# Kernel tuning notes

Hardware: AMD Instinct MI355X
Metric: run time of the kernel (lower is better)

The kernel has to match this reference:

```python
import jax, jax.numpy as jnp
import numpy as np

NEG = -1e20

def _rope(x):
    # x: (N, L, H, D). Original buffers use inv_freq over D with D/2 entries;
    # sin/cos tiled to full D to broadcast (original code's einsum was under-specified for 4D).
    L, D = x.shape[1], x.shape[3]
    inv_freq = 1.0 / (10000.0 ** (jnp.arange(0, D, 2, dtype=jnp.float32) / D))
    t = jnp.arange(L, dtype=jnp.float32)
    freqs = t[:, None] * inv_freq[None, :]            # (L, D/2)
    sin = jnp.concatenate([jnp.sin(freqs)] * 2, -1)[None, :, None, :]  # (1,L,1,D)
    cos = jnp.concatenate([jnp.cos(freqs)] * 2, -1)[None, :, None, :]
    return x * cos + jnp.flip(x, -1) * sin

def setup_inputs() -> dict:
    key = jax.random.key(0)
    ks = jax.random.split(key, 8)
    N, L, E, H = 2, 1024, 2048, 16
    D = E // H
    s = 0.02
    return {
        "values": jax.random.normal(ks[0], (N, L, E), jnp.float32),
        "keys": jax.random.normal(ks[1], (N, L, E), jnp.float32),
        "queries": jax.random.normal(ks[2], (N, L, E), jnp.float32),
        "mask": jax.random.randint(ks[3], (N, 1, L, L), 0, 2, jnp.int32),
        "Wv": jax.random.normal(ks[4], (D, D), jnp.float32) * s,
        "Wk": jax.random.normal(ks[5], (D, D), jnp.float32) * s,
        "Wq": jax.random.normal(ks[6], (D, D), jnp.float32) * s,
        "Wo": jax.random.normal(ks[7], (E, E), jnp.float32) * s,
        "bo": jnp.zeros((E,), jnp.float32),
    }

def reference(values, keys, queries, mask, Wv, Wk, Wq, Wo, bo):
    N, L, E = queries.shape
    H = 16
    D = E // H
    v = values.reshape(N, L, H, D)
    k = keys.reshape(N, L, H, D)
    q = queries.reshape(N, L, H, D)
    q = _rope(q)
    k = _rope(k)
    # per-head linears (nn.Linear: x @ W.T)
    v = jnp.einsum('nlhd,od->nlho', v, Wv)
    k = jnp.einsum('nlhd,od->nlho', k, Wk)
    q = jnp.einsum('nlhd,od->nlho', q, Wq)
    energy = jnp.einsum('nqhd,nkhd->nhqk', q, k)
    energy = jnp.where(mask == 0, NEG, energy)
    attn = jax.nn.softmax(energy / jnp.sqrt(jnp.float32(E)), axis=3)
    out = jnp.einsum('nhqk,nkhd->nqhd', attn, v).reshape(N, L, E)
    return out @ Wo.T + bo
```

## Files before the change

kernel.cpp:

```cpp
#include <hip/hip_runtime.h>

#define LQ 1024
#define EMB 2048
#define NH 16
#define HD 128
#define RSCALE 0.022097086912079608f

typedef unsigned short u16x8 __attribute__((ext_vector_type(8)));
typedef __bf16 bf16x8 __attribute__((ext_vector_type(8)));
typedef float f32x4 __attribute__((ext_vector_type(4)));
typedef short s16x4 __attribute__((ext_vector_type(4)));

typedef const __attribute__((address_space(1))) unsigned int* gas_t;
typedef __attribute__((address_space(3))) unsigned int* las_t;

__device__ __forceinline__ void glds16(const void* g, void* l){
  __builtin_amdgcn_global_load_lds((gas_t)g, (las_t)l, 16, 0, 0);
}
__device__ __forceinline__ unsigned short f2b(float f){
  unsigned int x = __float_as_uint(f);
  return (unsigned short)((x + 0x7fffu + ((x >> 16) & 1u)) >> 16);
}
__device__ __forceinline__ unsigned short f2bu(float f){
  union { __bf16 h; unsigned short u; } c; c.h = (__bf16)f; return c.u;
}
__device__ __forceinline__ short f2bs(float f){
  union { __bf16 h; short s; } c; c.h = (__bf16)f; return c.s;
}
__device__ __forceinline__ bf16x8 as_bf(u16x8 u){
  union { u16x8 u; bf16x8 b; } c; c.u = u; return c.b;
}
__device__ __forceinline__ f32x4 mfma16(s16x4 a, s16x4 b, f32x4 c){
  return __builtin_amdgcn_mfma_f32_16x16x16bf16_1k(a, b, c, 0, 0, 0);
}

__global__ __launch_bounds__(256) void k_proj(
    const float* __restrict__ vals, const float* __restrict__ keys,
    const float* __restrict__ qrys,
    const float* __restrict__ Wv, const float* __restrict__ Wk,
    const float* __restrict__ Wq,
    const float* __restrict__ Wo, const int* __restrict__ M,
    unsigned short* __restrict__ kp, unsigned short* __restrict__ qp,
    unsigned short* __restrict__ vtF, unsigned short* __restrict__ Wob,
    unsigned long long* __restrict__ Mb)
{
  __shared__ unsigned short Xs[64 * 136];
  __shared__ unsigned short Ws[128 * 136];
  __shared__ float scC[16 * 128], scS[16 * 128];
  int t = threadIdx.x;
  int which = blockIdx.y;

  if (which == 3) {
    int bx = blockIdx.x;
    #pragma unroll 4
    for (int k = 0; k < 32; ++k) {
      int i = (bx * 8192 + k * 256 + t) * 4;
      float4 f = *(const float4*)&Wo[i];
      ushort4 u;
      u.x = f2bu(f.x); u.y = f2bu(f.y); u.z = f2bu(f.z); u.w = f2bu(f.w);
      *(ushort4*)&Wob[i] = u;
    }
    int w = t >> 6, lane = t & 63;
    for (int i0 = 0; i0 < 64; i0 += 8) {
      int v[8];
      #pragma unroll
      for (int j = 0; j < 8; ++j) {
        int w_idx = bx * 256 + w * 64 + i0 + j;
        int n = w_idx >> 14, row = (w_idx >> 4) & 1023, wc = w_idx & 15;
        v[j] = M[(size_t)n * (LQ * LQ) + (size_t)row * LQ + wc * 64 + lane];
      }
      #pragma unroll
      for (int j = 0; j < 8; ++j) {
        unsigned long long b = __ballot(v[j] != 0);
        if (lane == 0) Mb[bx * 256 + w * 64 + i0 + j] = b;
      }
    }
    return;
  }

  const float* X; const float* W; bool rope;
  if (which == 0)      { X = vals; W = Wv; rope = false; }
  else if (which == 1) { X = keys; W = Wk; rope = true;  }
  else                 { X = qrys; W = Wq; rope = true;  }
  float qs = (which == 2) ? RSCALE : 1.0f;

  int w = t >> 6, lane = t & 63, quad = lane >> 4, n16 = lane & 15;

  #pragma unroll
  for (int i = 0; i < 8; ++i) {
    int ci = t + 256 * i;
    int row = ci >> 4, ch = ci & 15;
    float4 a = *(const float4*)&W[row * 128 + ch * 8];
    float4 b = *(const float4*)&W[row * 128 + ch * 8 + 4];
    u16x8 u;
    u[0]=f2bu(a.x); u[1]=f2bu(a.y); u[2]=f2bu(a.z); u[3]=f2bu(a.w);
    u[4]=f2bu(b.x); u[5]=f2bu(b.y); u[6]=f2bu(b.z); u[7]=f2bu(b.w);
    *(u16x8*)&Ws[row * 136 + ch * 8] = u;
  }
  if (rope) {
    int l0 = (blockIdx.x * 16) & 1023;
    #pragma unroll
    for (int i = 0; i < 8; ++i) {
      int idx = t + 256 * i;
      int li = idx >> 7, d = idx & 127, j = d & 63;
      float inv = 1.0f / powf(10000.0f, (float)(2 * j) * 0.0078125f);
      float ang = (float)(l0 + li) * inv;
      scC[idx] = cosf(ang);
      scS[idx] = sinf(ang);
    }
  }
  __syncthreads();

  int bh0 = blockIdx.x >> 2;
  for (int tile = 0; tile < 4; ++tile) {
    int bx4 = blockIdx.x * 4 + tile;
    int m0 = bx4 * 64;
    int kt0 = bx4 & 15;

    if (which == 0) {
      int n = bh0 >> 4, h = bh0 & 15;
      #pragma unroll
      for (int i = 0; i < 8; ++i) {
        int fi = t + 256 * i;
        int row = fi >> 5, dq = (fi & 31) * 4;
        size_t gr = (size_t)n * 16384 + (size_t)(kt0 * 64 + row) * 16 + h;
        float4 x = *(const float4*)&X[gr * HD + dq];
        ushort4 u;
        u.x = f2bu(x.x); u.y = f2bu(x.y); u.z = f2bu(x.z); u.w = f2bu(x.w);
        *(ushort4*)&Xs[row * 136 + dq] = u;
      }
    } else {
      #pragma unroll
      for (int i = 0; i < 8; ++i) {
        int fi = t + 256 * i;
        int row = fi >> 5, dq = (fi & 31) * 4;
        int gr = m0 + row;
        float4 x = *(const float4*)&X[(size_t)gr * HD + dq];
        int li = tile * 4 + (row >> 4);
        float4 xm = *(const float4*)&X[(size_t)gr * HD + (124 - dq)];
        float4 c  = *(const float4*)&scC[li * 128 + dq];
        float4 s  = *(const float4*)&scS[li * 128 + dq];
        ushort4 u;
        u.x = f2bu(x.x * c.x + xm.w * s.x);
        u.y = f2bu(x.y * c.y + xm.z * s.y);
        u.z = f2bu(x.z * c.z + xm.y * s.z);
        u.w = f2bu(x.w * c.w + xm.x * s.w);
        *(ushort4*)&Xs[row * 136 + dq] = u;
      }
    }
    __syncthreads();

    f32x4 of[4][2];
    #pragma unroll
    for (int a = 0; a < 4; ++a)
      { of[a][0] = (f32x4){0.f,0.f,0.f,0.f}; of[a][1] = (f32x4){0.f,0.f,0.f,0.f}; }

    #pragma unroll
    for (int kd = 0; kd < 4; ++kd) {
      bf16x8 bfr[2];
      #pragma unroll
      for (int b2 = 0; b2 < 2; ++b2)
        bfr[b2] = as_bf(*(const u16x8*)&Ws[(w * 32 + b2 * 16 + n16) * 136 + kd * 32 + quad * 8]);
      #pragma unroll
      for (int a = 0; a < 4; ++a) {
        bf16x8 af = as_bf(*(const u16x8*)&Xs[(a * 16 + n16) * 136 + kd * 32 + quad * 8]);
        of[a][0] = __builtin_amdgcn_mfma_f32_16x16x32_bf16(af, bfr[0], of[a][0], 0, 0, 0);
        of[a][1] = __builtin_amdgcn_mfma_f32_16x16x32_bf16(af, bfr[1], of[a][1], 0, 0, 0);
      }
    }

    if (which == 0) {
      size_t vbase = (size_t)bh0 * (LQ * HD) + (size_t)kt0 * 8192;
      #pragma unroll
      for (int a = 0; a < 4; ++a) {
        u16x8 u;
        u[0]=f2bu(of[a][0][0]); u[1]=f2bu(of[a][0][1]);
        u[2]=f2bu(of[a][0][2]); u[3]=f2bu(of[a][0][3]);
        u[4]=f2bu(of[a][1][0]); u[5]=f2bu(of[a][1][1]);
        u[6]=f2bu(of[a][1][2]); u[7]=f2bu(of[a][1][3]);
        *(u16x8*)&vtF[vbase + (size_t)(((a * 4 + w) * 64 + (quad * 16 + n16)) * 8)] = u;
      }
      __syncthreads();
    } else {
      unsigned short* OUT = (which == 1) ? kp : qp;
      __syncthreads();
      #pragma unroll
      for (int a = 0; a < 4; ++a)
        #pragma unroll
        for (int b2 = 0; b2 < 2; ++b2)
          #pragma unroll
          for (int r = 0; r < 4; ++r)
            Xs[(a * 16 + quad * 4 + r) * 136 + w * 32 + b2 * 16 + n16] =
                f2bu(of[a][b2][r] * qs);
      __syncthreads();
      #pragma unroll
      for (int i = 0; i < 4; ++i) {
        int chunk = t + 256 * i;
        int row = chunk >> 4, dc = chunk & 15;
        u16x8 v = *(const u16x8*)&Xs[row * 136 + dc * 8];
        int m = m0 + row;
        int n = m >> 14, l = (m >> 4) & 1023, h = m & 15;
        *(u16x8*)&OUT[(((size_t)(n * NH + h)) * LQ + l) * HD + dc * 8] = v;
      }
      __syncthreads();
    }
  }
}

__global__ __launch_bounds__(512) void k_attn(
    const unsigned short* __restrict__ qp, const unsigned short* __restrict__ kp,
    const unsigned short* __restrict__ vtF, const unsigned long long* __restrict__ Mb,
    unsigned short* __restrict__ ao)
{
  __shared__ unsigned short KsF[2][8192];
  __shared__ unsigned short VsF[2][8192];
  __shared__ float ls[8][16];
  int t = threadIdx.x, w = t >> 6, lane = t & 63, quad = lane >> 4, n16 = lane & 15;
  int grp = w >> 2, wq = w & 3;
  int lin = blockIdx.y * gridDim.x + blockIdx.x;
  int xcd = lin & 7, j = lin >> 3;
  int bh = xcd + 8 * (j >> 4);
  int q0 = (j & 15) * 64;
  int nIdx = bh >> 4, h = bh & 15;
  size_t base = (size_t)bh * LQ * HD;
  const unsigned short* Q = qp + base;
  const unsigned short* K = kp + base;
  const unsigned short* VF = vtF + base;

  bf16x8 qf[4];
  #pragma unroll
  for (int kd = 0; kd < 4; ++kd)
    qf[kd] = as_bf(*(const u16x8*)&Q[(size_t)(q0 + wq * 16 + n16) * HD + kd * 32 + quad * 8]);

  const unsigned long long* MbRow =
      Mb + ((size_t)nIdx * LQ + q0 + wq * 16 + n16) * 16;

  f32x4 of[8];
  #pragma unroll
  for (int c = 0; c < 8; ++c) of[c] = (f32x4){0.f, 0.f, 0.f, 0.f};
  float lp = 0.f;

  for (int p = 0; p < 8; ++p) {
    int k0 = p * 128;
    __syncthreads();
    #pragma unroll
    for (int jj = 0; jj < 2; ++jj) {
      int kt = 2 * p + jj;
      #pragma unroll
      for (int i = 0; i < 2; ++i) {
        int D = t + 512 * i;
        int nn = D & 15, qq = (D >> 4) & 3, cc = (D >> 6) & 3, kd = D >> 8;
        glds16(&K[(size_t)(k0 + jj * 64 + cc * 16 + nn) * HD + (kd * 4 + qq) * 8],
               &KsF[jj][(size_t)D * 8]);
        glds16(&VF[(size_t)kt * 8192 + (size_t)D * 8],
               &VsF[jj][(size_t)D * 8]);
      }
    }
    unsigned long long mq = MbRow[2 * p + grp];
    __syncthreads();

    unsigned long long msh = mq >> (quad * 4);

    f32x4 sf[4];
    #pragma unroll
    for (int c = 0; c < 4; ++c) sf[c] = (f32x4){0.f, 0.f, 0.f, 0.f};
    __builtin_amdgcn_s_setprio(1);
    #pragma unroll
    for (int kd = 0; kd < 4; ++kd) {
      #pragma unroll
      for (int c = 0; c < 4; ++c) {
        bf16x8 kv = as_bf(*(const u16x8*)&KsF[grp][((kd * 4 + c) * 64 + lane) * 8]);
        sf[c] = __builtin_amdgcn_mfma_f32_16x16x32_bf16(kv, qf[kd], sf[c], 0, 0, 0);
      }
    }
    __builtin_amdgcn_s_setprio(0);
    #pragma unroll
    for (int c = 0; c < 4; ++c) {
      s16x4 pa;
      #pragma unroll
      for (int r = 0; r < 4; ++r) {
        int bit = (int)((msh >> (c * 16 + r)) & 1ull);
        float p = bit ? __expf(sf[c][r]) : 0.f;
        lp += p;
        pa[r] = f2bs(p);
      }
      __builtin_amdgcn_s_setprio(1);
      #pragma unroll
      for (int c2p = 0; c2p < 4; ++c2p) {
        u16x8 vv2 = *(const u16x8*)&VsF[grp][((c * 4 + c2p) * 64 + lane) * 8];
        s16x4 vlo = { (short)vv2[0], (short)vv2[1], (short)vv2[2], (short)vv2[3] };
        s16x4 vhi = { (short)vv2[4], (short)vv2[5], (short)vv2[6], (short)vv2[7] };
        of[2 * c2p]     = mfma16(pa, vlo, of[2 * c2p]);
        of[2 * c2p + 1] = mfma16(pa, vhi, of[2 * c2p + 1]);
      }
      __builtin_amdgcn_s_setprio(0);
    }
  }

  __syncthreads();
  {
    float s = lp;
    s += __shfl_xor(s, 16);
    s += __shfl_xor(s, 32);
    ls[w][n16] = s;
  }
  float* OF = (float*)&KsF[0][0];
  unsigned short* AO = &VsF[0][0];
  if (grp == 1) {
    #pragma unroll
    for (int c2 = 0; c2 < 8; ++c2) {
      #pragma unroll
      for (int r = 0; r < 4; ++r) {
        OF[(wq * 16 + quad * 4 + r) * 128 + c2 * 16 + n16] = of[c2][r];
      }
    }
  }
  __syncthreads();
  if (grp == 0) {
    float linv[4];
    #pragma unroll
    for (int r = 0; r < 4; ++r)
      linv[r] = 1.0f / fmaxf(ls[wq][quad * 4 + r] + ls[wq + 4][quad * 4 + r], 1e-30f);
    #pragma unroll
    for (int c2 = 0; c2 < 8; ++c2) {
      #pragma unroll
      for (int r = 0; r < 4; ++r) {
        float v = of[c2][r] + OF[(wq * 16 + quad * 4 + r) * 128 + c2 * 16 + n16];
        AO[(wq * 16 + quad * 4 + r) * 128 + c2 * 16 + n16] = f2bu(v * linv[r]);
      }
    }
  }
  __syncthreads();
  #pragma unroll
  for (int i = 0; i < 2; ++i) {
    int chunk = t + 512 * i;
    int q = chunk >> 4, dc = chunk & 15;
    u16x8 v = *(const u16x8*)&AO[q * 128 + dc * 8];
    *(u16x8*)&ao[((size_t)(nIdx * LQ + q0 + q)) * EMB + h * HD + dc * 8] = v;
  }
}

__global__ __launch_bounds__(256) void k_outproj(
    const unsigned short* __restrict__ ao, const unsigned short* __restrict__ Wob,
    const float* __restrict__ bo, float* __restrict__ out)
{
  __shared__ unsigned short As[2][128 * 64];
  __shared__ unsigned short Bs[2][64 * 64];
  int t = threadIdx.x;
  int w = t >> 6, lane = t & 63, quad = lane >> 4, n16 = lane & 15;
  int wm = w >> 1, wo = w & 1;
  int m0 = blockIdx.x * 128, o0 = blockIdx.y * 64;
  int ub = (t & 192);

  f32x4 of[4][2];
  #pragma unroll
  for (int a = 0; a < 4; ++a)
    { of[a][0] = (f32x4){0.f,0.f,0.f,0.f}; of[a][1] = (f32x4){0.f,0.f,0.f,0.f}; }

  #pragma unroll
  for (int i = 0; i < 4; ++i) {
    int ci = t + 256 * i;
    int row = ci >> 3, ch = (ci & 7) ^ (row & 7);
    glds16(&ao[(size_t)(m0 + row) * EMB + ch * 8], &As[0][(ub + 256 * i) * 8]);
  }
  #pragma unroll
  for (int i = 0; i < 2; ++i) {
    int ci = t + 256 * i;
    int row = ci >> 3, ch = (ci & 7) ^ (row & 7);
    glds16(&Wob[(size_t)(o0 + row) * EMB + ch * 8], &Bs[0][(ub + 256 * i) * 8]);
  }

  for (int kt = 0; kt < 32; ++kt) {
    int cur = kt & 1;
    __syncthreads();
    if (kt < 31) {
      int k1 = (kt + 1) * 64;
      #pragma unroll
      for (int i = 0; i < 4; ++i) {
        int ci = t + 256 * i;
        int row = ci >> 3, ch = (ci & 7) ^ (row & 7);
        glds16(&ao[(size_t)(m0 + row) * EMB + k1 + ch * 8], &As[1 - cur][(ub + 256 * i) * 8]);
      }
      #pragma unroll
      for (int i = 0; i < 2; ++i) {
        int ci = t + 256 * i;
        int row = ci >> 3, ch = (ci & 7) ^ (row & 7);
        glds16(&Wob[(size_t)(o0 + row) * EMB + k1 + ch * 8], &Bs[1 - cur][(ub + 256 * i) * 8]);
      }
    }
    #pragma unroll
    for (int kd = 0; kd < 2; ++kd) {
      int slot0 = (kd * 4 + quad);
      bf16x8 af[4], bf[2];
      #pragma unroll
      for (int a = 0; a < 4; ++a)
        af[a] = as_bf(*(const u16x8*)&As[cur][(wm * 64 + a * 16 + n16) * 64 + (slot0 ^ (n16 & 7)) * 8]);
      #pragma unroll
      for (int b = 0; b < 2; ++b)
        bf[b] = as_bf(*(const u16x8*)&Bs[cur][(wo * 32 + b * 16 + n16) * 64 + (slot0 ^ (n16 & 7)) * 8]);
      #pragma unroll
      for (int a = 0; a < 4; ++a)
        #pragma unroll
        for (int b = 0; b < 2; ++b)
          of[a][b] = __builtin_amdgcn_mfma_f32_16x16x32_bf16(af[a], bf[b], of[a][b], 0, 0, 0);
    }
  }

  float bb[2] = { bo[o0 + wo * 32 + n16], bo[o0 + wo * 32 + 16 + n16] };
  #pragma unroll
  for (int a = 0; a < 4; ++a) {
    #pragma unroll
    for (int b = 0; b < 2; ++b) {
      #pragma unroll
      for (int r = 0; r < 4; ++r) {
        out[(size_t)(m0 + wm * 64 + a * 16 + quad * 4 + r) * EMB
            + o0 + wo * 32 + b * 16 + n16] = of[a][b][r] + bb[b];
      }
    }
  }
}

extern "C" void kernel_launch(void* const* d_in, const int* in_sizes, int n_in,
                              void* d_out, int out_size, void* d_ws, size_t ws_size,
                              hipStream_t stream) {
  (void)in_sizes; (void)n_in; (void)out_size; (void)ws_size;
  const float* vals = (const float*)d_in[0];
  const float* keys = (const float*)d_in[1];
  const float* qrys = (const float*)d_in[2];
  const int*   mask = (const int*)d_in[3];
  const float* Wv   = (const float*)d_in[4];
  const float* Wk   = (const float*)d_in[5];
  const float* Wq   = (const float*)d_in[6];
  const float* Wo   = (const float*)d_in[7];
  const float* bo   = (const float*)d_in[8];
  float* out = (float*)d_out;

  unsigned short* U  = (unsigned short*)d_ws;
  unsigned short* qp = U;
  unsigned short* kp = U + 4194304;
  unsigned short* vtF= U + 12582912;
  unsigned short* ao = U + 16777216;
  unsigned short* Wob= U + 20971520;
  unsigned long long* Mb = (unsigned long long*)(U + 25165824);

  k_proj    <<<dim3(128, 4), dim3(256), 0, stream>>>(vals, keys, qrys, Wv, Wk, Wq,
                                                     Wo, mask, kp, qp, vtF, Wob, Mb);
  k_attn    <<<dim3(16, 32), dim3(512), 0, stream>>>(qp, kp, vtF, Mb, ao);
  k_outproj <<<dim3(16, 32), dim3(256), 0, stream>>>(ao, Wob, bo, out);
}
```

Measured before the change: 188.1 us.

## Double-buffer K/V tiles with async LDS prefetch and split tiles across wave groups

```diff
diff --git a/kernel.cpp b/kernel.cpp
--- a/kernel.cpp
+++ b/kernel.cpp
@@ -240,54 +240,67 @@
   for (int c = 0; c < 8; ++c) of[c] = (f32x4){0.f, 0.f, 0.f, 0.f};
   float lp = 0.f;
 
-  for (int p = 0; p < 8; ++p) {
-    int k0 = p * 128;
-    __syncthreads();
-    #pragma unroll
-    for (int jj = 0; jj < 2; ++jj) {
-      int kt = 2 * p + jj;
+  #pragma unroll
+  for (int i = 0; i < 2; ++i) {
+    int D = t + 512 * i;
+    int nn = D & 15, qq = (D >> 4) & 3, cc = (D >> 6) & 3, kd = D >> 8;
+    glds16(&K[(size_t)(cc * 16 + nn) * HD + (kd * 4 + qq) * 8], &KsF[0][(size_t)D * 8]);
+    glds16(&VF[(size_t)D * 8], &VsF[0][(size_t)D * 8]);
+  }
+
+  for (int tt = 0; tt < 16; ++tt) {
+    int b = tt & 1;
+    __builtin_amdgcn_s_barrier();
+    unsigned long long mq = MbRow[tt];
+    if (tt < 15) {
+      int k0n = (tt + 1) * 64;
       #pragma unroll
       for (int i = 0; i < 2; ++i) {
         int D = t + 512 * i;
         int nn = D & 15, qq = (D >> 4) & 3, cc = (D >> 6) & 3, kd = D >> 8;
-        glds16(&K[(size_t)(k0 + jj * 64 + cc * 16 + nn) * HD + (kd * 4 + qq) * 8],
-               &KsF[jj][(size_t)D * 8]);
-        glds16(&VF[(size_t)kt * 8192 + (size_t)D * 8],
-               &VsF[jj][(size_t)D * 8]);
-      }
-    }
-    unsigned long long mq = MbRow[2 * p + grp];
-    __syncthreads();
-
-    unsigned long long msh = mq >> (quad * 4);
-
-    f32x4 sf[4];
-    #pragma unroll
-    for (int c = 0; c < 4; ++c) sf[c] = (f32x4){0.f, 0.f, 0.f, 0.f};
+        glds16(&K[(size_t)(k0n + cc * 16 + nn) * HD + (kd * 4 + qq) * 8],
+               &KsF[b ^ 1][(size_t)D * 8]);
+        glds16(&VF[(size_t)(tt + 1) * 8192 + (size_t)D * 8],
+               &VsF[b ^ 1][(size_t)D * 8]);
+      }
+      asm volatile("s_waitcnt vmcnt(4)" ::: "memory");
+    } else {
+      asm volatile("s_waitcnt vmcnt(0)" ::: "memory");
+    }
+    __builtin_amdgcn_s_barrier();
+    __builtin_amdgcn_sched_barrier(0);
+
+    unsigned long long msh = mq >> (grp * 32 + quad * 4);
+
+    f32x4 sf[2];
+    sf[0] = (f32x4){0.f, 0.f, 0.f, 0.f};
+    sf[1] = (f32x4){0.f, 0.f, 0.f, 0.f};
     __builtin_amdgcn_s_setprio(1);
     #pragma unroll
     for (int kd = 0; kd < 4; ++kd) {
       #pragma unroll
-      for (int c = 0; c < 4; ++c) {
-        bf16x8 kv = as_bf(*(const u16x8*)&KsF[grp][((kd * 4 + c) * 64 + lane) * 8]);
-        sf[c] = __builtin_amdgcn_mfma_f32_16x16x32_bf16(kv, qf[kd], sf[c], 0, 0, 0);
+      for (int ci = 0; ci < 2; ++ci) {
+        int c = 2 * grp + ci;
+        bf16x8 kv = as_bf(*(const u16x8*)&KsF[b][((kd * 4 + c) * 64 + lane) * 8]);
+        sf[ci] = __builtin_amdgcn_mfma_f32_16x16x32_bf16(kv, qf[kd], sf[ci], 0, 0, 0);
       }
     }
     __builtin_amdgcn_s_setprio(0);
     #pragma unroll
-    for (int c = 0; c < 4; ++c) {
+    for (int ci = 0; ci < 2; ++ci) {
+      int c = 2 * grp + ci;
       s16x4 pa;
       #pragma unroll
       for (int r = 0; r < 4; ++r) {
-        int bit = (int)((msh >> (c * 16 + r)) & 1ull);
-        float p = bit ? __expf(sf[c][r]) : 0.f;
+        int bit = (int)((msh >> (ci * 16 + r)) & 1ull);
+        float p = bit ? __expf(sf[ci][r]) : 0.f;
         lp += p;
         pa[r] = f2bs(p);
       }
       __builtin_amdgcn_s_setprio(1);
       #pragma unroll
       for (int c2p = 0; c2p < 4; ++c2p) {
-        u16x8 vv2 = *(const u16x8*)&VsF[grp][((c * 4 + c2p) * 64 + lane) * 8];
+        u16x8 vv2 = *(const u16x8*)&VsF[b][((c * 4 + c2p) * 64 + lane) * 8];
         s16x4 vlo = { (short)vv2[0], (short)vv2[1], (short)vv2[2], (short)vv2[3] };
         s16x4 vhi = { (short)vv2[4], (short)vv2[5], (short)vv2[6], (short)vv2[7] };
         of[2 * c2p]     = mfma16(pa, vlo, of[2 * c2p]);
```

New measurement: 191.1 us. No clear change (+1.6%).
